# Optimization experiments

Hardware: AMD Instinct MI355X
Metric: run time of the kernel (lower is better)

Reference implementation:

```python
import math
import jax, jax.numpy as jnp
import numpy as np

B, S, HID = 4, 2048, 1024
H, D = 16, 64  # num_head, head_dim
EPS = 1e-12  # F.normalize eps


def _qknorm(t, gamma):
    # t: [B, S, H, D]; F.normalize(dim=-1) * sqrt(D) * gamma[None]
    norm = jnp.sqrt(jnp.sum(t * t, axis=-1, keepdims=True))
    t = t / jnp.maximum(norm, EPS)
    return t * math.sqrt(D) * gamma  # gamma broadcasts over [B,S]


def setup_inputs() -> dict:
    key = jax.random.key(0)
    ks = jax.random.split(key, 8)
    s = 0.02
    return {
        "x": jax.random.normal(ks[0], (B, S, HID), jnp.float32),
        "q_w": jax.random.normal(ks[1], (HID, HID), jnp.float32) * s,
        "q_b": jnp.zeros((HID,), jnp.float32),
        "kv_w": jax.random.normal(ks[2], (2 * HID, HID), jnp.float32) * s,
        "kv_b": jnp.zeros((2 * HID,), jnp.float32),
        "gamma_q": jnp.ones((H, D), jnp.float32),
        "gamma_k": jnp.ones((H, D), jnp.float32),
        "out_w": jax.random.normal(ks[3], (HID, HID), jnp.float32) * s,
    }


def reference(x, q_w, q_b, kv_w, kv_b, gamma_q, gamma_k, out_w):
    # self-attention: context = x
    q = (x @ q_w.T + q_b).reshape(B, S, H, D)
    kv = x @ kv_w.T + kv_b  # [B, S, 2*HID]
    k, v = jnp.split(kv, 2, axis=-1)
    k = k.reshape(B, S, H, D)
    v = v.reshape(B, S, H, D)
    q = _qknorm(q, gamma_q)
    k = _qknorm(k, gamma_k)
    scores = jnp.einsum('bqhd,bkhd->bhqk', q, k)  # [B,H,S,S]
    attn = jax.nn.softmax(scores, axis=-1)
    out = jnp.einsum('bhqk,bkhd->bqhd', attn, v).reshape(B, S, HID)
    return out @ out_w.T
```

## Files before the change

kernel.cpp:

```cpp
#include <hip/hip_runtime.h>
#include <stdint.h>

#define B_ 4
#define S_ 2048
#define HID_ 1024
#define NH_ 16
#define HD_ 64

typedef __bf16 bf16x8 __attribute__((ext_vector_type(8)));
typedef __bf16 bf16x4 __attribute__((ext_vector_type(4)));
typedef float f32x4 __attribute__((ext_vector_type(4)));

__device__ inline void gload_lds16(const void* g, void* l) {
  __builtin_amdgcn_global_load_lds((const __attribute__((address_space(1))) unsigned int*)g,
                                   (__attribute__((address_space(3))) unsigned int*)l, 16, 0, 0);
}

__device__ inline f32x4 fmax4(f32x4 a, f32x4 b) {
  f32x4 r;
  r[0] = fmaxf(a[0], b[0]); r[1] = fmaxf(a[1], b[1]);
  r[2] = fmaxf(a[2], b[2]); r[3] = fmaxf(a[3], b[3]);
  return r;
}

__global__ __launch_bounds__(256) void cvt_bf16(const float* __restrict__ in, __bf16* __restrict__ out) {
  int i = (blockIdx.x * 256 + threadIdx.x) * 4;
  f32x4 v = *(const f32x4*)(in + i);
  bf16x4 o;
  o[0] = (__bf16)v[0]; o[1] = (__bf16)v[1]; o[2] = (__bf16)v[2]; o[3] = (__bf16)v[3];
  *(bf16x4*)(out + i) = o;
}

template <int MODE>
__global__ __launch_bounds__(256) void gemm_bt(const __bf16* __restrict__ A,
                                               const __bf16* __restrict__ Bt,
                                               const float* __restrict__ bias,
                                               const float* __restrict__ gamma,
                                               __bf16* __restrict__ Cb,
                                               float* __restrict__ Cf,
                                               __bf16* __restrict__ vt,
                                               int M, int N, int K) {
  const int n0 = blockIdx.x * 128;
  const int m0 = blockIdx.y * 128;
  const int tid  = threadIdx.x;
  const int wave = tid >> 6, lane = tid & 63;
  const int wm = wave >> 1, wn = wave & 1;
  const int lrow = lane & 15, lgrp = lane >> 4;

  __shared__ __bf16 sA[128][64];
  __shared__ __bf16 sB[128][64];

  f32x4 acc[4][4];
#pragma unroll
  for (int i = 0; i < 4; i++)
#pragma unroll
    for (int j = 0; j < 4; j++) acc[i][j] = f32x4{0.f, 0.f, 0.f, 0.f};

  for (int k0 = 0; k0 < K; k0 += 64) {
    __syncthreads();
#pragma unroll
    for (int c = 0; c < 4; c++) {
      const int row = wave * 32 + c * 8;
      const __bf16* ga = A + (size_t)(m0 + row + (lane >> 3)) * K + k0 + (lane & 7) * 8;
      gload_lds16(ga, &sA[row][0]);
      const __bf16* gb = Bt + (size_t)(n0 + row + (lane >> 3)) * K + k0 + (lane & 7) * 8;
      gload_lds16(gb, &sB[row][0]);
    }
    __syncthreads();
#pragma unroll
    for (int kk = 0; kk < 2; kk++) {
      bf16x8 af[4], bfr[4];
#pragma unroll
      for (int i = 0; i < 4; i++) {
        af[i]  = *(const bf16x8*)(&sA[wm * 64 + i * 16 + lrow][kk * 32 + 8 * lgrp]);
        bfr[i] = *(const bf16x8*)(&sB[wn * 64 + i * 16 + lrow][kk * 32 + 8 * lgrp]);
      }
#pragma unroll
      for (int i = 0; i < 4; i++)
#pragma unroll
        for (int j = 0; j < 4; j++)
          acc[i][j] = __builtin_amdgcn_mfma_f32_16x16x32_bf16(af[i], bfr[j], acc[i][j], 0, 0, 0);
    }
  }

  if (MODE != 1) {
    float bv[4];
#pragma unroll
    for (int j = 0; j < 4; j++) bv[j] = bias[n0 + wn * 64 + j * 16 + lrow];
#pragma unroll
    for (int i = 0; i < 4; i++)
#pragma unroll
      for (int j = 0; j < 4; j++)
#pragma unroll
        for (int r = 0; r < 4; r++) acc[i][j][r] += bv[j];
  }

  const bool do_norm = (MODE == 2) || (MODE == 3 && n0 < 1024);
  if (do_norm) {
    const float nscale = (MODE == 2) ? 8.f * 1.44269504f : 8.f;
    float g[4];
#pragma unroll
    for (int j = 0; j < 4; j++) g[j] = gamma[(n0 + wn * 64 + j * 16 + lrow) & 1023];
#pragma unroll
    for (int i = 0; i < 4; i++) {
#pragma unroll
      for (int r = 0; r < 4; r++) {
        float ss = acc[i][0][r] * acc[i][0][r] + acc[i][1][r] * acc[i][1][r] +
                   acc[i][2][r] * acc[i][2][r] + acc[i][3][r] * acc[i][3][r];
#pragma unroll
        for (int off = 1; off < 16; off <<= 1) ss += __shfl_xor(ss, off, 64);
        const float inv = nscale / fmaxf(sqrtf(ss), 1e-12f);
        const int m = m0 + wm * 64 + i * 16 + lgrp * 4 + r;
#pragma unroll
        for (int j = 0; j < 4; j++) {
          const int n = (n0 + wn * 64 + j * 16 + lrow) & 1023;
          Cb[(size_t)m * 1024 + n] = (__bf16)(acc[i][j][r] * inv * g[j]);
        }
      }
    }
  } else if (MODE == 3) {
#pragma unroll
    for (int i = 0; i < 4; i++) {
#pragma unroll
      for (int j = 0; j < 4; j++) {
        const int nn = n0 + wn * 64 + j * 16 + lrow - 1024;
        const int h = nn >> 6, d = nn & 63;
        const int m = m0 + wm * 64 + i * 16 + lgrp * 4;
        const int b = m >> 11, s0 = m & 2047;
        bf16x4 pk;
#pragma unroll
        for (int r = 0; r < 4; r++) pk[r] = (__bf16)acc[i][j][r];
        *(bf16x4*)(vt + ((size_t)((b * 16 + h) * 64 + d)) * 2048 + s0) = pk;
      }
    }
  } else {
#pragma unroll
    for (int i = 0; i < 4; i++)
#pragma unroll
      for (int j = 0; j < 4; j++) {
        const int n = n0 + wn * 64 + j * 16 + lrow;
#pragma unroll
        for (int r = 0; r < 4; r++) {
          const int m = m0 + wm * 64 + i * 16 + lgrp * 4 + r;
          Cf[(size_t)m * N + n] = acc[i][j][r];
        }
      }
  }
}

__global__ __launch_bounds__(512) void attn_kernel(const __bf16* __restrict__ qm,
                                                   const __bf16* __restrict__ km,
                                                   const __bf16* __restrict__ vtm,
                                                   __bf16* __restrict__ o) {
  constexpr float THR = 11.5416f;
  const int lin = blockIdx.y * gridDim.x + blockIdx.x;
  const int swz = (lin & 7) * 64 + (lin >> 3);
  const int qb = swz & 7;
  const int bh = swz >> 3;
  const int b = bh >> 4, h = bh & 15;
  const int q0 = qb * 256;
  const int tid = threadIdx.x, wave = tid >> 6, lane = tid & 63;
  const int lrow = lane & 15, lgrp = lane >> 4;

  __shared__ __bf16 sK[2][64 * 64];
  __shared__ __bf16 sVt[2][64 * 64];
  __shared__ __bf16 sP[8][2][16 * 64];

  const __bf16* kbase  = km + (size_t)(b * S_) * 1024 + h * 64;
  const __bf16* vtbase = vtm + (size_t)((b * 16 + h) * 64) * 2048;

  const int srow = lane >> 3;
  const int pchunk = lane & 7;

  auto stage = [&](int buf, int kt) {
    const int rr = wave * 8;
    const int r = rr + srow;
    gload_lds16(kbase + (size_t)(kt * 64 + r) * 1024 + ((pchunk ^ (r & 7)) << 3),
                &sK[buf][rr * 64]);
    gload_lds16(vtbase + (size_t)r * 2048 + kt * 64 + ((pchunk ^ (r & 7)) << 3),
                &sVt[buf][rr * 64]);
  };

  bf16x8 qf[2][2];
#pragma unroll
  for (int rt = 0; rt < 2; ++rt) {
    const __bf16* qp = qm + (size_t)(b * S_ + q0 + wave * 32 + rt * 16 + lrow) * 1024 + h * 64;
    qf[rt][0] = *(const bf16x8*)(qp + 8 * lgrp);
    qf[rt][1] = *(const bf16x8*)(qp + 32 + 8 * lgrp);
  }

  f32x4 accd[2][4];
#pragma unroll
  for (int rt = 0; rt < 2; ++rt)
#pragma unroll
    for (int dt = 0; dt < 4; ++dt) accd[rt][dt] = f32x4{0.f, 0.f, 0.f, 0.f};
  float m_r[2], l_r[2];
#pragma unroll
  for (int rt = 0; rt < 2; ++rt) { m_r[rt] = -1e30f; l_r[rt] = 0.f; }

  stage(0, 0);
  int buf = 0;
  for (int kt = 0; kt < S_ / 64; ++kt) {
    __syncthreads();
    if (kt + 1 < S_ / 64) stage(buf ^ 1, kt + 1);

    f32x4 sc[2][4];
#pragma unroll
    for (int rt = 0; rt < 2; ++rt)
#pragma unroll
      for (int t = 0; t < 4; ++t) sc[rt][t] = f32x4{0.f, 0.f, 0.f, 0.f};
    __builtin_amdgcn_s_setprio(1);
#pragma unroll
    for (int t = 0; t < 4; ++t) {
      const int krow = t * 16 + lrow;
#pragma unroll
      for (int kk = 0; kk < 2; ++kk) {
        bf16x8 kf = *(const bf16x8*)(&sK[buf][krow * 64 + (((kk * 4 + lgrp) ^ (krow & 7)) << 3)]);
        sc[0][t] = __builtin_amdgcn_mfma_f32_16x16x32_bf16(kf, qf[0][kk], sc[0][t], 0, 0, 0);
        sc[1][t] = __builtin_amdgcn_mfma_f32_16x16x32_bf16(kf, qf[1][kk], sc[1][t], 0, 0, 0);
      }
    }
    __builtin_amdgcn_s_setprio(0);

#pragma unroll
    for (int rt = 0; rt < 2; ++rt) {
      f32x4 mm = fmax4(fmax4(sc[rt][0], sc[rt][1]), fmax4(sc[rt][2], sc[rt][3]));
      float tm = fmaxf(fmaxf(mm[0], mm[1]), fmaxf(mm[2], mm[3]));
      tm = fmaxf(tm, __shfl_xor(tm, 16, 64));
      tm = fmaxf(tm, __shfl_xor(tm, 32, 64));

      if (!__all(tm - m_r[rt] <= THR)) {
        const float mn = fmaxf(m_r[rt], tm);
        const float scl = __builtin_exp2f(m_r[rt] - mn);
        m_r[rt] = mn;
        l_r[rt] *= scl;
        float sclr[4];
#pragma unroll
        for (int j = 0; j < 4; ++j) sclr[j] = __shfl(scl, lgrp * 4 + j, 64);
#pragma unroll
        for (int dt = 0; dt < 4; ++dt)
#pragma unroll
          for (int j = 0; j < 4; ++j) accd[rt][dt][j] *= sclr[j];
      }

      const float nm = m_r[rt];
      float ps0 = 0.f, ps1 = 0.f;
#pragma unroll
      for (int t = 0; t < 4; ++t) {
        bf16x4 pk;
        const float p0 = __builtin_exp2f(sc[rt][t][0] - nm);
        const float p1 = __builtin_exp2f(sc[rt][t][1] - nm);
        const float p2 = __builtin_exp2f(sc[rt][t][2] - nm);
        const float p3 = __builtin_exp2f(sc[rt][t][3] - nm);
        ps0 += p0 + p2; ps1 += p1 + p3;
        pk[0] = (__bf16)p0; pk[1] = (__bf16)p1; pk[2] = (__bf16)p2; pk[3] = (__bf16)p3;
        *(bf16x4*)(&sP[wave][rt][lrow * 64 + (((2 * t + (lgrp >> 1)) ^ (lrow & 7)) << 3) +
                                ((lgrp & 1) << 2)]) = pk;
      }
      float ps = ps0 + ps1;
      ps += __shfl_xor(ps, 16, 64);
      ps += __shfl_xor(ps, 32, 64);
      l_r[rt] += ps;
    }

    __builtin_amdgcn_s_setprio(1);
#pragma unroll
    for (int half = 0; half < 2; ++half) {
      bf16x8 vf[4];
#pragma unroll
      for (int dt = 0; dt < 4; ++dt) {
        const int d = dt * 16 + lrow;
        vf[dt] = *(const bf16x8*)(&sVt[buf][d * 64 + (((half * 4 + lgrp) ^ (lrow & 7)) << 3)]);
      }
#pragma unroll
      for (int rt = 0; rt < 2; ++rt) {
        bf16x8 pf = *(const bf16x8*)(&sP[wave][rt][lrow * 64 + (((half * 4 + lgrp) ^ (lrow & 7)) << 3)]);
#pragma unroll
        for (int dt = 0; dt < 4; ++dt)
          accd[rt][dt] = __builtin_amdgcn_mfma_f32_16x16x32_bf16(pf, vf[dt], accd[rt][dt], 0, 0, 0);
      }
    }
    __builtin_amdgcn_s_setprio(0);
    buf ^= 1;
  }

#pragma unroll
  for (int rt = 0; rt < 2; ++rt) {
#pragma unroll
    for (int j = 0; j < 4; ++j) {
      const float lv = __shfl(l_r[rt], lgrp * 4 + j, 64);
      const float inv = 1.f / lv;
      const int row = b * S_ + q0 + wave * 32 + rt * 16 + lgrp * 4 + j;
      __bf16* ob = o + (size_t)row * 1024 + h * 64;
#pragma unroll
      for (int dt = 0; dt < 4; ++dt) ob[dt * 16 + lrow] = (__bf16)(accd[rt][dt][j] * inv);
    }
  }
}

extern "C" void kernel_launch(void* const* d_in, const int* in_sizes, int n_in,
                              void* d_out, int out_size, void* d_ws, size_t ws_size,
                              hipStream_t stream) {
  (void)in_sizes; (void)n_in; (void)out_size; (void)ws_size;
  const float* x       = (const float*)d_in[0];
  const float* q_w     = (const float*)d_in[1];
  const float* q_b     = (const float*)d_in[2];
  const float* kv_w    = (const float*)d_in[3];
  const float* kv_b    = (const float*)d_in[4];
  const float* gamma_q = (const float*)d_in[5];
  const float* gamma_k = (const float*)d_in[6];
  const float* out_w   = (const float*)d_in[7];
  float* out = (float*)d_out;

  char* ws = (char*)d_ws;
  __bf16* x_bf   = (__bf16*)(ws);
  __bf16* qw_bf  = (__bf16*)(ws + (16ull << 20));
  __bf16* kvw_bf = (__bf16*)(ws + (18ull << 20));
  __bf16* ow_bf  = (__bf16*)(ws + (22ull << 20));
  __bf16* q_bf   = (__bf16*)(ws + (24ull << 20));
  __bf16* k_bf   = (__bf16*)(ws + (40ull << 20));
  __bf16* vt_bf  = (__bf16*)(ws + (56ull << 20));
  __bf16* at_bf  = (__bf16*)(ws + (72ull << 20));

  cvt_bf16<<<8192, 256, 0, stream>>>(x, x_bf);
  cvt_bf16<<<1024, 256, 0, stream>>>(q_w, qw_bf);
  cvt_bf16<<<2048, 256, 0, stream>>>(kv_w, kvw_bf);
  cvt_bf16<<<1024, 256, 0, stream>>>(out_w, ow_bf);

  gemm_bt<2><<<dim3(8, 64), 256, 0, stream>>>(x_bf, qw_bf, q_b, gamma_q, q_bf, nullptr, nullptr,
                                              8192, 1024, 1024);
  gemm_bt<3><<<dim3(16, 64), 256, 0, stream>>>(x_bf, kvw_bf, kv_b, gamma_k, k_bf, nullptr, vt_bf,
                                               8192, 2048, 1024);

  attn_kernel<<<dim3(8, 64), 512, 0, stream>>>(q_bf, k_bf, vt_bf, at_bf);

  gemm_bt<1><<<dim3(8, 64), 256, 0, stream>>>(at_bf, ow_bf, nullptr, nullptr, nullptr, out, nullptr,
                                              8192, 1024, 1024);
}
```

Measured before the change: 344.2 us.

## Fuse Q and KV projection GEMMs and interleave attention PV per row tile

Concatenates the Q and KV weights so a single GEMM launch computes Q, K and V, with per-column-block epilogues for normalization or the V transpose. This removes one launch and the tail between the two projection GEMMs. In the attention kernel, the P·V MFMAs now run right after each row tile's softmax, so the P shared buffer shrinks by half. That lowers LDS use but reloads V fragments per row tile.

```diff
diff --git a/kernel.cpp b/kernel.cpp
--- a/kernel.cpp
+++ b/kernel.cpp
@@ -34,9 +34,12 @@
 template <int MODE>
 __global__ __launch_bounds__(256) void gemm_bt(const __bf16* __restrict__ A,
                                                const __bf16* __restrict__ Bt,
-                                               const float* __restrict__ bias,
-                                               const float* __restrict__ gamma,
-                                               __bf16* __restrict__ Cb,
+                                               const float* __restrict__ bias_q,
+                                               const float* __restrict__ bias_kv,
+                                               const float* __restrict__ gamma_q,
+                                               const float* __restrict__ gamma_k,
+                                               __bf16* __restrict__ Cq,
+                                               __bf16* __restrict__ Ck,
                                                float* __restrict__ Cf,
                                                __bf16* __restrict__ vt,
                                                int M, int N, int K) {
@@ -83,54 +86,59 @@
     }
   }
 
-  if (MODE != 1) {
+  if (MODE == 4) {
     float bv[4];
 #pragma unroll
-    for (int j = 0; j < 4; j++) bv[j] = bias[n0 + wn * 64 + j * 16 + lrow];
+    for (int j = 0; j < 4; j++) {
+      const int n = n0 + wn * 64 + j * 16 + lrow;
+      bv[j] = (n < 1024) ? bias_q[n] : bias_kv[n - 1024];
+    }
 #pragma unroll
     for (int i = 0; i < 4; i++)
 #pragma unroll
       for (int j = 0; j < 4; j++)
 #pragma unroll
         for (int r = 0; r < 4; r++) acc[i][j][r] += bv[j];
-  }
-
-  const bool do_norm = (MODE == 2) || (MODE == 3 && n0 < 1024);
-  if (do_norm) {
-    const float nscale = (MODE == 2) ? 8.f * 1.44269504f : 8.f;
-    float g[4];
-#pragma unroll
-    for (int j = 0; j < 4; j++) g[j] = gamma[(n0 + wn * 64 + j * 16 + lrow) & 1023];
-#pragma unroll
-    for (int i = 0; i < 4; i++) {
-#pragma unroll
-      for (int r = 0; r < 4; r++) {
-        float ss = acc[i][0][r] * acc[i][0][r] + acc[i][1][r] * acc[i][1][r] +
-                   acc[i][2][r] * acc[i][2][r] + acc[i][3][r] * acc[i][3][r];
-#pragma unroll
-        for (int off = 1; off < 16; off <<= 1) ss += __shfl_xor(ss, off, 64);
-        const float inv = nscale / fmaxf(sqrtf(ss), 1e-12f);
-        const int m = m0 + wm * 64 + i * 16 + lgrp * 4 + r;
+
+    const int nblk = n0 >> 10;
+    if (nblk < 2) {
+      const float nscale = (nblk == 0) ? 8.f * 1.44269504f : 8.f;
+      const float* gam = (nblk == 0) ? gamma_q : gamma_k;
+      __bf16* dst = (nblk == 0) ? Cq : Ck;
+      float g[4];
+#pragma unroll
+      for (int j = 0; j < 4; j++) g[j] = gam[(n0 + wn * 64 + j * 16 + lrow) & 1023];
+#pragma unroll
+      for (int i = 0; i < 4; i++) {
+#pragma unroll
+        for (int r = 0; r < 4; r++) {
+          float ss = acc[i][0][r] * acc[i][0][r] + acc[i][1][r] * acc[i][1][r] +
+                     acc[i][2][r] * acc[i][2][r] + acc[i][3][r] * acc[i][3][r];
+#pragma unroll
+          for (int off = 1; off < 16; off <<= 1) ss += __shfl_xor(ss, off, 64);
+          const float inv = nscale / fmaxf(sqrtf(ss), 1e-12f);
+          const int m = m0 + wm * 64 + i * 16 + lgrp * 4 + r;
+#pragma unroll
+          for (int j = 0; j < 4; j++) {
+            const int n = (n0 + wn * 64 + j * 16 + lrow) & 1023;
+            dst[(size_t)m * 1024 + n] = (__bf16)(acc[i][j][r] * inv * g[j]);
+          }
+        }
+      }
+    } else {
+#pragma unroll
+      for (int i = 0; i < 4; i++) {
 #pragma unroll
         for (int j = 0; j < 4; j++) {
-          const int n = (n0 + wn * 64 + j * 16 + lrow) & 1023;
-          Cb[(size_t)m * 1024 + n] = (__bf16)(acc[i][j][r] * inv * g[j]);
+          const int nn = n0 + wn * 64 + j * 16 + lrow - 2048;
+          const int h = nn >> 6, d = nn & 63;
+          const int m = m0 + wm * 64 + i * 16 + lgrp * 4;
+          const int b = m >> 11, s0 = m & 2047;
+          bf16x4 pk;
+#pragma unroll
+          for (int r = 0; r < 4; r++) pk[r] = (__bf16)acc[i][j][r];
+          *(bf16x4*)(vt + ((size_t)((b * 16 + h) * 64 + d)) * 2048 + s0) = pk;
         }
-      }
-    }
-  } else if (MODE == 3) {
-#pragma unroll
-    for (int i = 0; i < 4; i++) {
-#pragma unroll
-      for (int j = 0; j < 4; j++) {
-        const int nn = n0 + wn * 64 + j * 16 + lrow - 1024;
-        const int h = nn >> 6, d = nn & 63;
-        const int m = m0 + wm * 64 + i * 16 + lgrp * 4;
-        const int b = m >> 11, s0 = m & 2047;
-        bf16x4 pk;
-#pragma unroll
-        for (int r = 0; r < 4; r++) pk[r] = (__bf16)acc[i][j][r];
-        *(bf16x4*)(vt + ((size_t)((b * 16 + h) * 64 + d)) * 2048 + s0) = pk;
       }
     }
   } else {
@@ -164,7 +172,7 @@
 
   __shared__ __bf16 sK[2][64 * 64];
   __shared__ __bf16 sVt[2][64 * 64];
-  __shared__ __bf16 sP[8][2][16 * 64];
+  __shared__ __bf16 sP[8][16 * 64];
 
   const __bf16* kbase  = km + (size_t)(b * S_) * 1024 + h * 64;
   const __bf16* vtbase = vtm + (size_t)((b * 16 + h) * 64) * 2048;
@@ -254,33 +262,27 @@
         const float p3 = __builtin_exp2f(sc[rt][t][3] - nm);
         ps0 += p0 + p2; ps1 += p1 + p3;
         pk[0] = (__bf16)p0; pk[1] = (__bf16)p1; pk[2] = (__bf16)p2; pk[3] = (__bf16)p3;
-        *(bf16x4*)(&sP[wave][rt][lrow * 64 + (((2 * t + (lgrp >> 1)) ^ (lrow & 7)) << 3) +
-                                ((lgrp & 1) << 2)]) = pk;
+        *(bf16x4*)(&sP[wave][lrow * 64 + (((2 * t + (lgrp >> 1)) ^ (lrow & 7)) << 3) +
+                             ((lgrp & 1) << 2)]) = pk;
       }
       float ps = ps0 + ps1;
       ps += __shfl_xor(ps, 16, 64);
       ps += __shfl_xor(ps, 32, 64);
       l_r[rt] += ps;
-    }
-
-    __builtin_amdgcn_s_setprio(1);
-#pragma unroll
-    for (int half = 0; half < 2; ++half) {
-      bf16x8 vf[4];
-#pragma unroll
-      for (int dt = 0; dt < 4; ++dt) {
-        const int d = dt * 16 + lrow;
-        vf[dt] = *(const bf16x8*)(&sVt[buf][d * 64 + (((half * 4 + lgrp) ^ (lrow & 7)) << 3)]);
-      }
-#pragma unroll
-      for (int rt = 0; rt < 2; ++rt) {
-        bf16x8 pf = *(const bf16x8*)(&sP[wave][rt][lrow * 64 + (((half * 4 + lgrp) ^ (lrow & 7)) << 3)]);
-#pragma unroll
-        for (int dt = 0; dt < 4; ++dt)
-          accd[rt][dt] = __builtin_amdgcn_mfma_f32_16x16x32_bf16(pf, vf[dt], accd[rt][dt], 0, 0, 0);
-      }
-    }
-    __builtin_amdgcn_s_setprio(0);
+
+      __builtin_amdgcn_s_setprio(1);
+#pragma unroll
+      for (int half = 0; half < 2; ++half) {
+        bf16x8 pf = *(const bf16x8*)(&sP[wave][lrow * 64 + (((half * 4 + lgrp) ^ (lrow & 7)) << 3)]);
+#pragma unroll
+        for (int dt = 0; dt < 4; ++dt) {
+          const int d = dt * 16 + lrow;
+          bf16x8 vf = *(const bf16x8*)(&sVt[buf][d * 64 + (((half * 4 + lgrp) ^ (d & 7)) << 3)]);
+          accd[rt][dt] = __builtin_amdgcn_mfma_f32_16x16x32_bf16(pf, vf, accd[rt][dt], 0, 0, 0);
+        }
+      }
+      __builtin_amdgcn_s_setprio(0);
+    }
     buf ^= 1;
   }
 
@@ -314,8 +316,7 @@
 
   char* ws = (char*)d_ws;
   __bf16* x_bf   = (__bf16*)(ws);
-  __bf16* qw_bf  = (__bf16*)(ws + (16ull << 20));
-  __bf16* kvw_bf = (__bf16*)(ws + (18ull << 20));
+  __bf16* qkvw_bf = (__bf16*)(ws + (16ull << 20));
   __bf16* ow_bf  = (__bf16*)(ws + (22ull << 20));
   __bf16* q_bf   = (__bf16*)(ws + (24ull << 20));
   __bf16* k_bf   = (__bf16*)(ws + (40ull << 20));
@@ -323,17 +324,15 @@
   __bf16* at_bf  = (__bf16*)(ws + (72ull << 20));
 
   cvt_bf16<<<8192, 256, 0, stream>>>(x, x_bf);
-  cvt_bf16<<<1024, 256, 0, stream>>>(q_w, qw_bf);
-  cvt_bf16<<<2048, 256, 0, stream>>>(kv_w, kvw_bf);
+  cvt_bf16<<<1024, 256, 0, stream>>>(q_w, qkvw_bf);
+  cvt_bf16<<<2048, 256, 0, stream>>>(kv_w, qkvw_bf + (1024ull * 1024));
   cvt_bf16<<<1024, 256, 0, stream>>>(out_w, ow_bf);
 
-  gemm_bt<2><<<dim3(8, 64), 256, 0, stream>>>(x_bf, qw_bf, q_b, gamma_q, q_bf, nullptr, nullptr,
-                                              8192, 1024, 1024);
-  gemm_bt<3><<<dim3(16, 64), 256, 0, stream>>>(x_bf, kvw_bf, kv_b, gamma_k, k_bf, nullptr, vt_bf,
-                                               8192, 2048, 1024);
+  gemm_bt<4><<<dim3(24, 64), 256, 0, stream>>>(x_bf, qkvw_bf, q_b, kv_b, gamma_q, gamma_k,
+                                               q_bf, k_bf, nullptr, vt_bf, 8192, 3072, 1024);
 
   attn_kernel<<<dim3(8, 64), 512, 0, stream>>>(q_bf, k_bf, vt_bf, at_bf);
 
-  gemm_bt<1><<<dim3(8, 64), 256, 0, stream>>>(at_bf, ow_bf, nullptr, nullptr, nullptr, out, nullptr,
-                                              8192, 1024, 1024);
-}
+  gemm_bt<1><<<dim3(8, 64), 256, 0, stream>>>(at_bf, ow_bf, nullptr, nullptr, nullptr, nullptr,
+                                              nullptr, nullptr, out, nullptr, 8192, 1024, 1024);
+}
```

New measurement: 341.2 us. About the same (-0.9%).
